# Kernel tuning notes

Hardware: AMD Instinct MI355X
Metric: run time of the kernel (lower is better)

## Reference

```python
import jax, jax.numpy as jnp
import numpy as np
import math

B, S, E = 2, 2048, 1024
H, HD = 16, 64
FF = 4 * E
EPS = float(jnp.finfo(jnp.float32).eps)  # torch nn.RMSNorm default eps


def setup_inputs() -> dict:
    key = jax.random.key(0)
    ks = jax.random.split(key, 20)
    sd = 0.02
    inp = {
        "x": jax.random.normal(ks[0], (B, S, E), jnp.float32),
        "wq": jax.random.normal(ks[1], (E, H * HD), jnp.float32) * sd,
        "bq": jnp.zeros((H * HD,), jnp.float32),
        "wk": jax.random.normal(ks[2], (E, HD), jnp.float32) * sd,
        "bk": jnp.zeros((HD,), jnp.float32),
        "wv": jax.random.normal(ks[3], (E, HD), jnp.float32) * sd,
        "bv": jnp.zeros((HD,), jnp.float32),
        "wo": jax.random.normal(ks[4], (H * HD, E), jnp.float32) * sd,
        "bo": jnp.zeros((E,), jnp.float32),
        "wg": jax.random.normal(ks[5], (E, FF), jnp.float32) * sd,
        "bg": jnp.zeros((FF,), jnp.float32),
        "wu": jax.random.normal(ks[6], (E, FF), jnp.float32) * sd,
        "bu": jnp.zeros((FF,), jnp.float32),
        "wd": jax.random.normal(ks[7], (FF, E), jnp.float32) * sd,
        "bd": jnp.zeros((E,), jnp.float32),
        "g1": jnp.ones((E,), jnp.float32),
        "g2": jnp.ones((E,), jnp.float32),
    }
    return inp


def rmsnorm(x, g):
    ms = jnp.mean(jnp.square(x), axis=-1, keepdims=True)
    return x * jax.lax.rsqrt(ms + EPS) * g


def apply_rope(t):
    # t: [B, H, S, D]; llama-style rotate-half, theta=10000, start_pos=0
    d = t.shape[-1]
    half = d // 2
    inv_freq = 1.0 / (10000.0 ** (jnp.arange(half, dtype=jnp.float32) / half))
    pos = jnp.arange(t.shape[2], dtype=jnp.float32)
    ang = pos[:, None] * inv_freq[None, :]  # [S, half]
    cos, sin = jnp.cos(ang), jnp.sin(ang)
    t1, t2 = t[..., :half], t[..., half:]
    return jnp.concatenate([t1 * cos - t2 * sin, t1 * sin + t2 * cos], axis=-1)


def decoder_fwd(x, wq, bq, wk, bk, wv, bv, wo, bo, wg, bg, wu, bu, wd, bd, g1, g2):
    residual = x
    h = rmsnorm(x, g1)
    # MQA projections: H query heads, 1 shared K/V head
    q = (h @ wq + bq).reshape(B, S, H, HD).transpose(0, 2, 1, 3)  # [B,H,S,D]
    k = (h @ wk + bk)[:, None]                                    # [B,1,S,D]
    v = (h @ wv + bv)                                             # [B,S,D]
    q = apply_rope(q)
    k = apply_rope(k)[:, 0]                                       # [B,S,D]
    scores = jnp.einsum("bhqd,bkd->bhqk", q, k) / math.sqrt(HD)
    causal = jnp.tril(jnp.ones((S, S), dtype=bool))
    scores = jnp.where(causal, scores, -jnp.inf)
    attn = jax.nn.softmax(scores, axis=-1)
    out = jnp.einsum("bhqk,bkd->bhqd", attn, v)
    out = out.transpose(0, 2, 1, 3).reshape(B, S, H * HD)
    x = (out @ wo + bo) + residual
    residual = x
    h = rmsnorm(x, g2)
    gated = jax.nn.gelu(h @ wg + bg, approximate=False)  # torch GELU is exact erf
    up = h @ wu + bu
    x = (up * gated) @ wd + bd
    return x + residual


def reference(x, wq, bq, wk, bk, wv, bv, wo, bo, wg, bg, wu, bu, wd, bd, g1, g2):
    return decoder_fwd(x, wq, bq, wk, bk, wv, bv, wo, bo, wg, bg, wu, bu, wd, bd, g1, g2)
```

## Files before the change

kernel.cpp:

```cpp
#include <hip/hip_runtime.h>
#include <hip/hip_bf16.h>
#include <math.h>

#define BB 2
#define SS 2048
#define EE 1024
#define HH 16
#define HD 64
#define FFF 4096
#define MROWS (BB * SS)
#define EPS_F 1.1920929e-7f
#define NQKV 1152

typedef __hip_bfloat16 bf16;
typedef __attribute__((ext_vector_type(8))) short short8;
typedef __attribute__((ext_vector_type(4))) short short4v;
typedef __attribute__((ext_vector_type(4))) float floatx4;

typedef const __attribute__((address_space(1))) void* gas_t;
typedef __attribute__((address_space(3))) void* las_t;

#define BAR __builtin_amdgcn_s_barrier()
#define WLG do { asm volatile("s_waitcnt lgkmcnt(0)" ::: "memory"); \
                 __builtin_amdgcn_sched_barrier(0); } while (0)
#define VMC(N) asm volatile("s_waitcnt vmcnt(" #N ")" ::: "memory")

__global__ __launch_bounds__(256) void rmsnorm_kernel(const float* __restrict__ x,
                                                      const float* __restrict__ g,
                                                      bf16* __restrict__ out,
                                                      int cols) {
    int row = blockIdx.x;
    const float* xr = x + (size_t)row * cols;
    float ss = 0.0f;
    for (int c = threadIdx.x; c < cols; c += 256) {
        float v = xr[c];
        ss += v * v;
    }
    for (int off = 32; off > 0; off >>= 1) ss += __shfl_xor(ss, off, 64);
    __shared__ float red[4];
    int wave = threadIdx.x >> 6;
    if ((threadIdx.x & 63) == 0) red[wave] = ss;
    __syncthreads();
    float tot = red[0] + red[1] + red[2] + red[3];
    float rs = rsqrtf(tot / (float)cols + EPS_F);
    bf16* orow = out + (size_t)row * cols;
    for (int c = threadIdx.x; c < cols; c += 256) {
        orow[c] = __float2bfloat16(xr[c] * rs * g[c]);
    }
}

__global__ __launch_bounds__(256) void transpose_cast_kernel(const float* __restrict__ W,
                                                             bf16* __restrict__ Wt,
                                                             int K, int N) {
    __shared__ float t[32][33];
    int n0 = blockIdx.x * 32, k0 = blockIdx.y * 32;
    int tx = threadIdx.x & 31, ty = threadIdx.x >> 5;
#pragma unroll
    for (int i = 0; i < 4; ++i) {
        int kk = ty + i * 8;
        t[kk][tx] = W[(size_t)(k0 + kk) * N + n0 + tx];
    }
    __syncthreads();
#pragma unroll
    for (int i = 0; i < 4; ++i) {
        int nn = ty + i * 8;
        Wt[(size_t)(n0 + nn) * K + k0 + tx] = __float2bfloat16(t[tx][nn]);
    }
}

__global__ __launch_bounds__(256) void pack_bqkv_kernel(const float* __restrict__ bq,
                                                        const float* __restrict__ bk,
                                                        const float* __restrict__ bv,
                                                        float* __restrict__ bqkv) {
    int t = blockIdx.x * 256 + threadIdx.x;
    if (t >= NQKV) return;
    float v;
    if (t < 1024)      v = bq[t];
    else if (t < 1088) v = bk[t - 1024];
    else               v = bv[t - 1088];
    bqkv[t] = v;
}

#define GK 64

__global__ __launch_bounds__(256) void gemm_qkv_kernel(
        const bf16* __restrict__ A, const bf16* __restrict__ Bt,
        const float* __restrict__ bias,
        bf16* __restrict__ qout, float* __restrict__ kvout, int K) {
    __shared__ short As[128 * GK];
    __shared__ short Bs[128 * GK];
    int tid = threadIdx.x;
    int wave = tid >> 6, lane = tid & 63;
    int wm = (wave >> 1) * 64, wn = (wave & 1) * 64;
    int row0 = blockIdx.y * 128, col0 = blockIdx.x * 128;
    int lr = lane & 15, lq = lane >> 4;

    int srow = wave * 32 + (lane >> 3);
    int scol = (lane & 7) * 8;
    const bf16* Abase = A + (size_t)(row0 + srow) * K + scol;
    const bf16* Bbase = Bt + (size_t)(col0 + srow) * K + scol;

    floatx4 acc[4][4];
#pragma unroll
    for (int mi = 0; mi < 4; ++mi)
#pragma unroll
        for (int ni = 0; ni < 4; ++ni)
            acc[mi][ni] = (floatx4){0.f, 0.f, 0.f, 0.f};

    for (int k0 = 0; k0 < K; k0 += GK) {
        __syncthreads();
#pragma unroll
        for (int c = 0; c < 4; ++c) {
            __builtin_amdgcn_global_load_lds(
                (gas_t)(Abase + (size_t)(c * 8) * K + k0),
                (las_t)&As[(wave * 32 + c * 8) * GK], 16, 0, 0);
            __builtin_amdgcn_global_load_lds(
                (gas_t)(Bbase + (size_t)(c * 8) * K + k0),
                (las_t)&Bs[(wave * 32 + c * 8) * GK], 16, 0, 0);
        }
        __syncthreads();
#pragma unroll
        for (int ks = 0; ks < GK; ks += 32) {
            short8 af[4], bfr[4];
#pragma unroll
            for (int mi = 0; mi < 4; ++mi)
                af[mi] = *(const short8*)&As[(wm + mi * 16 + lr) * GK + ks + lq * 8];
#pragma unroll
            for (int ni = 0; ni < 4; ++ni)
                bfr[ni] = *(const short8*)&Bs[(wn + ni * 16 + lr) * GK + ks + lq * 8];
#pragma unroll
            for (int mi = 0; mi < 4; ++mi)
#pragma unroll
                for (int ni = 0; ni < 4; ++ni)
                    acc[mi][ni] = __builtin_amdgcn_mfma_f32_16x16x32_bf16(
                        af[mi], bfr[ni], acc[mi][ni], 0, 0, 0);
        }
    }

#pragma unroll
    for (int mi = 0; mi < 4; ++mi) {
#pragma unroll
        for (int ni = 0; ni < 4; ++ni) {
            int gc = col0 + wn + ni * 16 + lr;
            float bv = bias[gc];
#pragma unroll
            for (int r = 0; r < 4; ++r) {
                int gr = row0 + wm + mi * 16 + lq * 4 + r;
                float c = acc[mi][ni][r] + bv;
                if (gc < 1024) qout[(size_t)gr * 1024 + gc] = __float2bfloat16(c);
                else           kvout[(size_t)gr * 128 + (gc - 1024)] = c;
            }
        }
    }
}

__global__ __launch_bounds__(256) void gemm_n64_kernel(
        const bf16* __restrict__ A, const bf16* __restrict__ Bt,
        const float* __restrict__ bias, const float* __restrict__ aux,
        float* __restrict__ C, int M, int N, int K) {
    __shared__ short As[128 * GK];
    __shared__ short Bs[64 * GK];
    int tid = threadIdx.x;
    int wave = tid >> 6, lane = tid & 63;
    int wm = wave * 32;
    int row0 = blockIdx.y * 128, col0 = blockIdx.x * 64;
    int lr = lane & 15, lq = lane >> 4;

    int srow = (lane >> 3);
    int scol = (lane & 7) * 8;
    const bf16* Abase = A + (size_t)(row0 + wave * 32 + srow) * K + scol;
    const bf16* Bbase = Bt + (size_t)(col0 + wave * 16 + srow) * K + scol;

    floatx4 acc[2][4];
#pragma unroll
    for (int mi = 0; mi < 2; ++mi)
#pragma unroll
        for (int ni = 0; ni < 4; ++ni)
            acc[mi][ni] = (floatx4){0.f, 0.f, 0.f, 0.f};

    for (int k0 = 0; k0 < K; k0 += GK) {
        __syncthreads();
#pragma unroll
        for (int c = 0; c < 4; ++c)
            __builtin_amdgcn_global_load_lds(
                (gas_t)(Abase + (size_t)(c * 8) * K + k0),
                (las_t)&As[(wave * 32 + c * 8) * GK], 16, 0, 0);
#pragma unroll
        for (int c = 0; c < 2; ++c)
            __builtin_amdgcn_global_load_lds(
                (gas_t)(Bbase + (size_t)(c * 8) * K + k0),
                (las_t)&Bs[(wave * 16 + c * 8) * GK], 16, 0, 0);
        __syncthreads();
#pragma unroll
        for (int ks = 0; ks < GK; ks += 32) {
            short8 af[2], bfr[4];
#pragma unroll
            for (int mi = 0; mi < 2; ++mi)
                af[mi] = *(const short8*)&As[(wm + mi * 16 + lr) * GK + ks + lq * 8];
#pragma unroll
            for (int ni = 0; ni < 4; ++ni)
                bfr[ni] = *(const short8*)&Bs[(ni * 16 + lr) * GK + ks + lq * 8];
#pragma unroll
            for (int mi = 0; mi < 2; ++mi)
#pragma unroll
                for (int ni = 0; ni < 4; ++ni)
                    acc[mi][ni] = __builtin_amdgcn_mfma_f32_16x16x32_bf16(
                        af[mi], bfr[ni], acc[mi][ni], 0, 0, 0);
        }
    }

#pragma unroll
    for (int mi = 0; mi < 2; ++mi) {
#pragma unroll
        for (int ni = 0; ni < 4; ++ni) {
            int gc = col0 + ni * 16 + lr;
            float bv = bias[gc];
#pragma unroll
            for (int r = 0; r < 4; ++r) {
                int gr = row0 + wm + mi * 16 + lq * 4 + r;
                size_t idx = (size_t)gr * N + gc;
                C[idx] = acc[mi][ni][r] + bv + aux[idx];
            }
        }
    }
}

#define FFN_RD_A(KH, MH) \
    { const short* Ap = &Ab[buf][KH][0]; \
      af[0] = *(const short8*)&Ap[(wr * 128 + ((MH) * 4 + 0) * 16 + lr) * 32 + cs8]; \
      af[1] = *(const short8*)&Ap[(wr * 128 + ((MH) * 4 + 1) * 16 + lr) * 32 + cs8]; \
      af[2] = *(const short8*)&Ap[(wr * 128 + ((MH) * 4 + 2) * 16 + lr) * 32 + cs8]; \
      af[3] = *(const short8*)&Ap[(wr * 128 + ((MH) * 4 + 3) * 16 + lr) * 32 + cs8]; }

#define FFN_RD_B(KH) \
    { const short* Bp = &Bb[buf][KH][0]; \
      gf[0] = *(const short8*)&Bp[(wc * 32 + lr) * 32 + cs8]; \
      gf[1] = *(const short8*)&Bp[(wc * 32 + 16 + lr) * 32 + cs8]; \
      uf[0] = *(const short8*)&Bp[4096 + (wc * 32 + lr) * 32 + cs8]; \
      uf[1] = *(const short8*)&Bp[4096 + (wc * 32 + 16 + lr) * 32 + cs8]; }

#define FFN_MM(MH) \
    __builtin_amdgcn_s_setprio(1); \
    { _Pragma("unroll") for (int mi = 0; mi < 4; ++mi) { \
        ag[(MH) * 4 + mi][0] = __builtin_amdgcn_mfma_f32_16x16x32_bf16(af[mi], gf[0], ag[(MH) * 4 + mi][0], 0, 0, 0); \
        ag[(MH) * 4 + mi][1] = __builtin_amdgcn_mfma_f32_16x16x32_bf16(af[mi], gf[1], ag[(MH) * 4 + mi][1], 0, 0, 0); \
        au[(MH) * 4 + mi][0] = __builtin_amdgcn_mfma_f32_16x16x32_bf16(af[mi], uf[0], au[(MH) * 4 + mi][0], 0, 0, 0); \
        au[(MH) * 4 + mi][1] = __builtin_amdgcn_mfma_f32_16x16x32_bf16(af[mi], uf[1], au[(MH) * 4 + mi][1], 0, 0, 0); } } \
    __builtin_amdgcn_s_setprio(0);

__global__ __launch_bounds__(512, 2) void gemm_ffn_kernel(
        const bf16* __restrict__ A, const bf16* __restrict__ Bg,
        const bf16* __restrict__ Bu, const float* __restrict__ biasg,
        const float* __restrict__ biasu, bf16* __restrict__ C, int K) {
    __shared__ short Ab[2][2][8192];
    __shared__ short Bb[2][2][8192];

    const int tid = threadIdx.x;
    const int w = tid >> 6, lane = tid & 63;
    const int wr = w >> 2, wc = w & 3;
    const int lr = lane & 15, quad = lane >> 4;
    const int row0 = blockIdx.y * 256, col0 = blockIdx.x * 128;
    const int NT = K >> 6;
    const int cs8 = (quad ^ ((lr >> 1) & 3)) * 8;

    const int sr = tid >> 2;
    const int scs = (((tid & 3) ^ ((tid >> 3) & 3))) * 8;

    auto stageA = [&](short* dst, int kcol) {
        __builtin_amdgcn_global_load_lds(
            (gas_t)(A + (size_t)(row0 + sr) * K + kcol + scs),
            (las_t)(dst + tid * 8), 16, 0, 0);
        __builtin_amdgcn_global_load_lds(
            (gas_t)(A + (size_t)(row0 + 128 + sr) * K + kcol + scs),
            (las_t)(dst + 4096 + tid * 8), 16, 0, 0);
    };
    auto stageB = [&](short* dst, int kcol) {
        __builtin_amdgcn_global_load_lds(
            (gas_t)(Bg + (size_t)(col0 + sr) * K + kcol + scs),
            (las_t)(dst + tid * 8), 16, 0, 0);
        __builtin_amdgcn_global_load_lds(
            (gas_t)(Bu + (size_t)(col0 + sr) * K + kcol + scs),
            (las_t)(dst + 4096 + tid * 8), 16, 0, 0);
    };

    floatx4 ag[8][2], au[8][2];
#pragma unroll
    for (int mi = 0; mi < 8; ++mi)
#pragma unroll
        for (int ni = 0; ni < 2; ++ni) {
            ag[mi][ni] = (floatx4){0.f, 0.f, 0.f, 0.f};
            au[mi][ni] = (floatx4){0.f, 0.f, 0.f, 0.f};
        }

    stageA(&Ab[0][0][0], 0);
    stageB(&Bb[0][0][0], 0);
    stageA(&Ab[0][1][0], 32);
    stageB(&Bb[0][1][0], 32);
    stageA(&Ab[1][0][0], 64);
    stageB(&Bb[1][0][0], 64);
    VMC(8);
    BAR;

    for (int k = 0; k < NT; ++k) {
        const int buf = k & 1;
        short8 gf[2], uf[2];
        {
            short8 af[4];
            FFN_RD_A(0, 0)
            FFN_RD_B(0)
            if (k + 1 < NT) stageA(&Ab[buf ^ 1][1][0], (k + 1) * 64 + 32);
            BAR; WLG;
            FFN_MM(0)
            BAR;
        }
        {
            short8 af[4];
            FFN_RD_A(0, 1)
            if (k + 1 < NT) stageB(&Bb[buf ^ 1][1][0], (k + 1) * 64 + 32);
            BAR; WLG;
            FFN_MM(1)
            if (k < NT - 1) { VMC(8); } else { VMC(0); }
            BAR;
        }
        {
            short8 af[4];
            FFN_RD_A(1, 0)
            FFN_RD_B(1)
            if (k + 2 < NT) stageA(&Ab[buf][0][0], (k + 2) * 64);
            BAR; WLG;
            FFN_MM(0)
            BAR;
        }
        {
            short8 af[4];
            FFN_RD_A(1, 1)
            if (k + 2 < NT) stageB(&Bb[buf][0][0], (k + 2) * 64);
            BAR; WLG;
            FFN_MM(1)
            if (k < NT - 2) { VMC(8); } else if (k == NT - 2) { VMC(4); }
            BAR;
        }
    }

#pragma unroll
    for (int mi = 0; mi < 8; ++mi) {
#pragma unroll
        for (int ni = 0; ni < 2; ++ni) {
            int gc = col0 + wc * 32 + ni * 16 + lr;
            float bg_ = biasg[gc], bu_ = biasu[gc];
#pragma unroll
            for (int r = 0; r < 4; ++r) {
                int gr = row0 + wr * 128 + mi * 16 + quad * 4 + r;
                float g = ag[mi][ni][r] + bg_;
                float u = au[mi][ni][r] + bu_;
                float v = 0.5f * g * (1.0f + erff(g * 0.70710678118654752f)) * u;
                C[(size_t)gr * FFF + gc] = __float2bfloat16(v);
            }
        }
    }
}

__global__ __launch_bounds__(256) void rope_table_kernel(float* __restrict__ ct,
                                                         float* __restrict__ st) {
    int idx = blockIdx.x * 256 + threadIdx.x;
    int i = idx & 31, s = idx >> 5;
    float inv = powf(10000.0f, -(float)i / 32.0f);
    float ang = (float)s * inv;
    ct[idx] = cosf(ang);
    st[idx] = sinf(ang);
}

__global__ __launch_bounds__(256) void rope_q_kernel(bf16* __restrict__ t,
                                                     const float* __restrict__ ct,
                                                     const float* __restrict__ st,
                                                     int total) {
    int idx = blockIdx.x * 256 + threadIdx.x;
    if (idx >= total) return;
    int i = idx & 31;
    int h = (idx >> 5) % HH;
    int row = idx / (32 * HH);
    int s = row & (SS - 1);
    float c = ct[s * 32 + i];
    float sn = st[s * 32 + i];
    size_t base = (size_t)row * (HH * HD) + h * 64 + i;
    float t1 = (float)t[base];
    float t2 = (float)t[base + 32];
    t[base]      = __float2bfloat16((t1 * c - t2 * sn) * 0.125f);
    t[base + 32] = __float2bfloat16((t1 * sn + t2 * c) * 0.125f);
}

__global__ __launch_bounds__(256) void prep_kv_kernel(const float* __restrict__ kv,
                                                      const float* __restrict__ ct,
                                                      const float* __restrict__ st,
                                                      bf16* __restrict__ kbf,
                                                      bf16* __restrict__ vtb) {
    __shared__ float vt[64][65];
    int s0 = blockIdx.x * 64;
    int b  = blockIdx.y;
    int tid = threadIdx.x;

    for (int i = tid; i < 2048; i += 256) {
        int sl = i >> 5, ii = i & 31;
        int s = s0 + sl;
        size_t base = ((size_t)(b * SS + s)) * 128;
        float k1 = kv[base + ii], k2 = kv[base + ii + 32];
        float c = ct[s * 32 + ii];
        float sn = st[s * 32 + ii];
        size_t ob = ((size_t)(b * SS + s)) * 64;
        kbf[ob + ii]      = __float2bfloat16(k1 * c - k2 * sn);
        kbf[ob + ii + 32] = __float2bfloat16(k1 * sn + k2 * c);
    }

    for (int i = tid; i < 4096; i += 256) {
        int s = i >> 6, d = i & 63;
        vt[d][s] = kv[((size_t)(b * SS + s0 + s)) * 128 + 64 + d];
    }
    __syncthreads();
    for (int i = tid; i < 4096; i += 256) {
        int d = i >> 6, sl = i & 63;
        vtb[((size_t)(b * 64 + d)) * SS + s0 + sl] = __float2bfloat16(vt[d][sl]);
    }
}

#define PST 68
#define SM_SHIFT 6.0f

__global__ __launch_bounds__(256, 3) void attn_mfma_kernel(
        const bf16* __restrict__ q, const bf16* __restrict__ kb,
        const bf16* __restrict__ vt,
        float* __restrict__ O0p, float* __restrict__ O1p,
        float* __restrict__ l0p, float* __restrict__ l1p) {
    __shared__ short Kb_s[2][64 * 64];
    __shared__ short Vb_s[2][64 * 64];
    __shared__ short Ps[4][16 * PST];

    int h = blockIdx.y, b = blockIdx.z;
    int px = blockIdx.x >> 1, half = blockIdx.x & 1;
    int tid = threadIdx.x, w = tid >> 6, lane = tid & 63;
    int lr = lane & 15, quad = lane >> 4;
    int rsw = lane & 7;

    float* __restrict__ Op = half ? O1p : O0p;
    float* __restrict__ lp = half ? l1p : l0p;

    const bf16* kbB = kb + (size_t)b * SS * 64;
    const bf16* vtB = vt + (size_t)b * 64 * SS;

    int st_sub = lane >> 3;
    int st_col = ((lane & 7) ^ st_sub) << 3;

    auto stage_tile = [&](int nxt, int j0s) {
#pragma unroll
        for (int i = 0; i < 2; ++i) {
            int rr = i * 32 + w * 8 + st_sub;
            __builtin_amdgcn_global_load_lds(
                (gas_t)(kbB + (size_t)(j0s + rr) * 64 + st_col),
                (las_t)&Kb_s[nxt][(i * 256 + w * 64) * 8], 16, 0, 0);
            __builtin_amdgcn_global_load_lds(
                (gas_t)(vtB + (size_t)rr * SS + j0s + st_col),
                (las_t)&Vb_s[nxt][(i * 256 + w * 64) * 8], 16, 0, 0);
        }
    };

    for (int pass = 0; pass < 2; ++pass) {
        int qt = (pass == 0) ? px : (SS / 64 - 1 - px);
        int q0 = qt * 64;

        const bf16* qrow = q + ((size_t)(b * SS + q0 + w * 16 + lr)) * (HH * HD) + h * HD;
        short8 qf0 = *(const short8*)(qrow + quad * 8);
        short8 qf1 = *(const short8*)(qrow + 32 + quad * 8);

        int n  = qt + 1;
        int n0 = (n + 1) >> 1;
        int tlo = half ? n0 : 0;
        int thi = half ? n  : n0;

        floatx4 O[4];
#pragma unroll
        for (int ni = 0; ni < 4; ++ni) O[ni] = (floatx4){0.f, 0.f, 0.f, 0.f};
        float lrow[4] = {0.f, 0.f, 0.f, 0.f};

        int cur = 0;
        if (tlo < thi) stage_tile(0, tlo * 64);
        __syncthreads();

        for (int t = tlo; t < thi; ++t) {
            if (t + 1 < thi) stage_tile(cur ^ 1, (t + 1) * 64);

            int j0 = t * 64;

            floatx4 S[4];
#pragma unroll
            for (int ni = 0; ni < 4; ++ni) S[ni] = (floatx4){0.f, 0.f, 0.f, 0.f};
#pragma unroll
            for (int ni = 0; ni < 4; ++ni) {
                const short* Kc = &Kb_s[cur][(ni * 16 + lr) * 64];
                short8 b0 = *(const short8*)&Kc[(quad ^ rsw) * 8];
                short8 b1 = *(const short8*)&Kc[((quad ^ rsw) ^ 4) * 8];
                S[ni] = __builtin_amdgcn_mfma_f32_16x16x32_bf16(qf0, b0, S[ni], 0, 0, 0);
                S[ni] = __builtin_amdgcn_mfma_f32_16x16x32_bf16(qf1, b1, S[ni], 0, 0, 0);
            }

            short8 vf[8];
#pragma unroll
            for (int ni = 0; ni < 4; ++ni) {
                const short* Vc = &Vb_s[cur][(ni * 16 + lr) * 64];
                vf[2 * ni]     = *(const short8*)&Vc[(quad ^ rsw) * 8];
                vf[2 * ni + 1] = *(const short8*)&Vc[((quad ^ rsw) ^ 4) * 8];
            }

            if (t == qt) {
                int rowg = q0 + w * 16 + quad * 4;
#pragma unroll
                for (int ni = 0; ni < 4; ++ni) {
                    int colg = j0 + ni * 16 + lr;
#pragma unroll
                    for (int r = 0; r < 4; ++r)
                        if (colg > rowg + r) S[ni][r] = -3.0e38f;
                }
            }

#pragma unroll
            for (int ni = 0; ni < 4; ++ni)
#pragma unroll
                for (int r = 0; r < 4; ++r)
                    S[ni][r] = __expf(S[ni][r] - SM_SHIFT);
#pragma unroll
            for (int r = 0; r < 4; ++r)
                lrow[r] += S[0][r] + S[1][r] + S[2][r] + S[3][r];

#pragma unroll
            for (int ni = 0; ni < 4; ++ni)
#pragma unroll
                for (int r = 0; r < 4; ++r) {
                    bf16 pb = __float2bfloat16(S[ni][r]);
                    Ps[w][(quad * 4 + r) * PST + ni * 16 + lr] = *(short*)&pb;
                }
            short4v a0 = *(const short4v*)&Ps[w][lr * PST + quad * 8];
            short4v a1 = *(const short4v*)&Ps[w][lr * PST + quad * 8 + 4];
            short4v a2 = *(const short4v*)&Ps[w][lr * PST + 32 + quad * 8];
            short4v a3 = *(const short4v*)&Ps[w][lr * PST + 32 + quad * 8 + 4];
            short8 p0 = __builtin_shufflevector(a0, a1, 0, 1, 2, 3, 4, 5, 6, 7);
            short8 p1 = __builtin_shufflevector(a2, a3, 0, 1, 2, 3, 4, 5, 6, 7);

#pragma unroll
            for (int ni = 0; ni < 4; ++ni) {
                O[ni] = __builtin_amdgcn_mfma_f32_16x16x32_bf16(p0, vf[2 * ni], O[ni], 0, 0, 0);
                O[ni] = __builtin_amdgcn_mfma_f32_16x16x32_bf16(p1, vf[2 * ni + 1], O[ni], 0, 0, 0);
            }

            __syncthreads();
            cur ^= 1;
        }

#pragma unroll
        for (int r = 0; r < 4; ++r) {
            float l = lrow[r];
            for (int off = 1; off < 16; off <<= 1) l += __shfl_xor(l, off, 64);
            lrow[r] = l;
        }

#pragma unroll
        for (int ni = 0; ni < 4; ++ni) {
            int gc = h * 64 + ni * 16 + lr;
#pragma unroll
            for (int r = 0; r < 4; ++r) {
                int gr = b * SS + q0 + w * 16 + quad * 4 + r;
                Op[(size_t)gr * (HH * HD) + gc] = O[ni][r];
            }
        }
        if (lr == 0) {
#pragma unroll
            for (int r = 0; r < 4; ++r) {
                int gr = b * SS + q0 + w * 16 + quad * 4 + r;
                lp[(size_t)gr * HH + h] = lrow[r];
            }
        }
    }
}

__global__ __launch_bounds__(256) void attn_combine_kernel(
        const float* __restrict__ O0p, const float* __restrict__ O1p,
        const float* __restrict__ l0p, const float* __restrict__ l1p,
        bf16* __restrict__ o) {
    int idx = blockIdx.x * 256 + threadIdx.x;
    int d4  = idx & 15;
    int hh  = (idx >> 4) & 15;
    int row = idx >> 8;
    float l = l0p[row * HH + hh] + l1p[row * HH + hh];
    float inv = 1.0f / l;
    size_t base = (size_t)row * (HH * HD) + hh * 64 + d4 * 4;
    float4 a = *(const float4*)(O0p + base);
    float4 c = *(const float4*)(O1p + base);
    short4v o4;
    {
        bf16 v0 = __float2bfloat16((a.x + c.x) * inv);
        bf16 v1 = __float2bfloat16((a.y + c.y) * inv);
        bf16 v2 = __float2bfloat16((a.z + c.z) * inv);
        bf16 v3 = __float2bfloat16((a.w + c.w) * inv);
        o4[0] = *(short*)&v0; o4[1] = *(short*)&v1;
        o4[2] = *(short*)&v2; o4[3] = *(short*)&v3;
    }
    *(short4v*)(o + base) = o4;
}

#define MB (1024ull * 1024ull)

extern "C" void kernel_launch(void* const* d_in, const int* in_sizes, int n_in,
                              void* d_out, int out_size, void* d_ws, size_t ws_size,
                              hipStream_t stream) {
    const float* x  = (const float*)d_in[0];
    const float* wq = (const float*)d_in[1];
    const float* bq = (const float*)d_in[2];
    const float* wk = (const float*)d_in[3];
    const float* bk = (const float*)d_in[4];
    const float* wv = (const float*)d_in[5];
    const float* bv = (const float*)d_in[6];
    const float* wo = (const float*)d_in[7];
    const float* bo = (const float*)d_in[8];
    const float* wg = (const float*)d_in[9];
    const float* bg = (const float*)d_in[10];
    const float* wu = (const float*)d_in[11];
    const float* bu = (const float*)d_in[12];
    const float* wd = (const float*)d_in[13];
    const float* bd = (const float*)d_in[14];
    const float* g1 = (const float*)d_in[15];
    const float* g2 = (const float*)d_in[16];
    float* out = (float*)d_out;

    char* ws = (char*)d_ws;
    bf16*  qbf   = (bf16*)(ws);
    bf16*  wuT   = (bf16*)(ws + 8 * MB);
    float* x2    = (float*)(ws + 16 * MB);
    bf16*  h1b   = (bf16*)(ws + 32 * MB);
    float* kv    = (float*)(ws + 40 * MB);
    bf16*  ao    = (bf16*)(ws + 42 * MB);
    bf16*  gg    = (bf16*)(ws + 50 * MB);
    bf16*  kbf   = (bf16*)(ws + 50 * MB);
    bf16*  vtb   = (bf16*)(ws + 50 * MB + 512 * 1024);
    float* Opart0 = (float*)(ws + 16 * MB);
    float* Opart1 = (float*)(ws + 51 * MB);
    float* lpart0 = (float*)(ws + 67 * MB);
    float* lpart1 = (float*)(ws + 67 * MB + 256 * 1024);
    float* ctab   = (float*)(ws + 68 * MB);
    float* stab   = (float*)(ws + 68 * MB + 256 * 1024);
    bf16*  wqkvT = (bf16*)(ws + 82 * MB);
    float* bqkv  = (float*)(ws + 84 * MB + 512 * 1024);
    bf16*  woT   = (bf16*)(ws + 85 * MB);
    bf16*  wgT   = (bf16*)(ws);
    bf16*  wdT   = (bf16*)(ws + 42 * MB);
    bf16*  h2b   = h1b;

    rmsnorm_kernel<<<MROWS, 256, 0, stream>>>(x, g1, h1b, EE);

    transpose_cast_kernel<<<dim3(EE / 32, EE / 32), 256, 0, stream>>>(wq, wqkvT, EE, EE);
    transpose_cast_kernel<<<dim3(HD / 32, EE / 32), 256, 0, stream>>>(wk, wqkvT + (size_t)1024 * EE, EE, HD);
    transpose_cast_kernel<<<dim3(HD / 32, EE / 32), 256, 0, stream>>>(wv, wqkvT + (size_t)1088 * EE, EE, HD);
    pack_bqkv_kernel<<<(NQKV + 255) / 256, 256, 0, stream>>>(bq, bk, bv, bqkv);
    transpose_cast_kernel<<<dim3(EE / 32, EE / 32), 256, 0, stream>>>(wo, woT, EE, EE);

    gemm_qkv_kernel<<<dim3(NQKV / 128, MROWS / 128), 256, 0, stream>>>(
        h1b, wqkvT, bqkv, qbf, kv, EE);

    rope_table_kernel<<<(SS * 32) / 256, 256, 0, stream>>>(ctab, stab);

    {
        int total_q = MROWS * HH * 32;
        rope_q_kernel<<<(total_q + 255) / 256, 256, 0, stream>>>(qbf, ctab, stab, total_q);
    }
    prep_kv_kernel<<<dim3(SS / 64, BB), 256, 0, stream>>>(kv, ctab, stab, kbf, vtb);

    attn_mfma_kernel<<<dim3(2 * SS / 128, HH, BB), 256, 0, stream>>>(
        qbf, kbf, vtb, Opart0, Opart1, lpart0, lpart1);
    attn_combine_kernel<<<(MROWS * HH * HD / 4) / 256, 256, 0, stream>>>(
        Opart0, Opart1, lpart0, lpart1, ao);

    gemm_n64_kernel<<<dim3(EE / 64, MROWS / 128), 256, 0, stream>>>(
        ao, woT, bo, x, x2, MROWS, EE, EE);

    rmsnorm_kernel<<<MROWS, 256, 0, stream>>>(x2, g2, h2b, EE);

    transpose_cast_kernel<<<dim3(FFF / 32, EE / 32), 256, 0, stream>>>(wg, wgT, EE, FFF);
    transpose_cast_kernel<<<dim3(FFF / 32, EE / 32), 256, 0, stream>>>(wu, wuT, EE, FFF);

    gemm_ffn_kernel<<<dim3(FFF / 128, MROWS / 256), 512, 0, stream>>>(
        h2b, wgT, wuT, bg, bu, gg, EE);

    transpose_cast_kernel<<<dim3(EE / 32, FFF / 32), 256, 0, stream>>>(wd, wdT, FFF, EE);
    gemm_n64_kernel<<<dim3(EE / 64, MROWS / 128), 256, 0, stream>>>(
        gg, wdT, bd, x2, out, MROWS, EE, FFF);
}
```

Before: 429.0 us.

## Fuse RoPE into QKV GEMM epilogue and batch weight-prep kernels

Applies rotary embedding, including the q scale, directly in the QKV GEMM epilogue. Each wave's 64-column slice is one head, so the rotate-half pairs are already in registers; this removes the separate q RoPE pass and the fp32 K/V intermediate. K and V are now written straight out as bf16, and a slimmer kernel only transposes V. All attention and FFN weight transposes, bias packing and the RoPE table build are merged into two multi-role launches, cutting launch count and small-kernel tail overhead. The trade-off is a heavier, more branchy GEMM epilogue that does scattered cos/sin table loads.

New measurement: 415.3 us. 3.2% less time.

```diff
diff --git a/kernel.cpp b/kernel.cpp
--- a/kernel.cpp
+++ b/kernel.cpp
@@ -49,12 +49,12 @@
     }
 }
 
-__global__ __launch_bounds__(256) void transpose_cast_kernel(const float* __restrict__ W,
-                                                             bf16* __restrict__ Wt,
-                                                             int K, int N) {
-    __shared__ float t[32][33];
-    int n0 = blockIdx.x * 32, k0 = blockIdx.y * 32;
-    int tx = threadIdx.x & 31, ty = threadIdx.x >> 5;
+__device__ __forceinline__ void transpose_tile32(const float* __restrict__ W,
+                                                 bf16* __restrict__ Wt,
+                                                 int K, int N, int bx, int by,
+                                                 int tid, float (*t)[33]) {
+    int n0 = bx * 32, k0 = by * 32;
+    int tx = tid & 31, ty = tid >> 5;
 #pragma unroll
     for (int i = 0; i < 4; ++i) {
         int kk = ty + i * 8;
@@ -68,17 +68,60 @@
     }
 }
 
-__global__ __launch_bounds__(256) void pack_bqkv_kernel(const float* __restrict__ bq,
-                                                        const float* __restrict__ bk,
-                                                        const float* __restrict__ bv,
-                                                        float* __restrict__ bqkv) {
-    int t = blockIdx.x * 256 + threadIdx.x;
-    if (t >= NQKV) return;
-    float v;
-    if (t < 1024)      v = bq[t];
-    else if (t < 1088) v = bk[t - 1024];
-    else               v = bv[t - 1088];
-    bqkv[t] = v;
+__global__ __launch_bounds__(256) void prep_weights_kernel(
+        const float* __restrict__ wq, const float* __restrict__ wk,
+        const float* __restrict__ wv, const float* __restrict__ wo,
+        const float* __restrict__ bq, const float* __restrict__ bk,
+        const float* __restrict__ bv,
+        bf16* __restrict__ wqkvT, bf16* __restrict__ woT,
+        float* __restrict__ bqkv, float* __restrict__ ct, float* __restrict__ st) {
+    __shared__ float t[32][33];
+    int bid = blockIdx.x, tid = threadIdx.x;
+    if (bid < 1024) {
+        transpose_tile32(wq, wqkvT, EE, EE, bid & 31, bid >> 5, tid, t);
+    } else if (bid < 1088) {
+        int b2 = bid - 1024;
+        transpose_tile32(wk, wqkvT + (size_t)1024 * EE, EE, HD, b2 & 1, b2 >> 1, tid, t);
+    } else if (bid < 1152) {
+        int b2 = bid - 1088;
+        transpose_tile32(wv, wqkvT + (size_t)1088 * EE, EE, HD, b2 & 1, b2 >> 1, tid, t);
+    } else if (bid < 2176) {
+        int b2 = bid - 1152;
+        transpose_tile32(wo, woT, EE, EE, b2 & 31, b2 >> 5, tid, t);
+    } else if (bid < 2432) {
+        int idx = (bid - 2176) * 256 + tid;
+        int i = idx & 31, s = idx >> 5;
+        float inv = powf(10000.0f, -(float)i / 32.0f);
+        float ang = (float)s * inv;
+        ct[idx] = cosf(ang);
+        st[idx] = sinf(ang);
+    } else {
+        int tt = (bid - 2432) * 256 + tid;
+        if (tt < NQKV) {
+            float v;
+            if (tt < 1024)      v = bq[tt];
+            else if (tt < 1088) v = bk[tt - 1024];
+            else                v = bv[tt - 1088];
+            bqkv[tt] = v;
+        }
+    }
+}
+
+__global__ __launch_bounds__(256) void ffn_weights_kernel(
+        const float* __restrict__ wg, const float* __restrict__ wu,
+        const float* __restrict__ wd,
+        bf16* __restrict__ wgT, bf16* __restrict__ wuT, bf16* __restrict__ wdT) {
+    __shared__ float t[32][33];
+    int bid = blockIdx.x, tid = threadIdx.x;
+    if (bid < 4096) {
+        transpose_tile32(wg, wgT, EE, FFF, bid & 127, bid >> 7, tid, t);
+    } else if (bid < 8192) {
+        int b2 = bid - 4096;
+        transpose_tile32(wu, wuT, EE, FFF, b2 & 127, b2 >> 7, tid, t);
+    } else {
+        int b2 = bid - 8192;
+        transpose_tile32(wd, wdT, FFF, EE, b2 & 31, b2 >> 5, tid, t);
+    }
 }
 
 #define GK 64
@@ -86,7 +129,9 @@
 __global__ __launch_bounds__(256) void gemm_qkv_kernel(
         const bf16* __restrict__ A, const bf16* __restrict__ Bt,
         const float* __restrict__ bias,
-        bf16* __restrict__ qout, float* __restrict__ kvout, int K) {
+        const float* __restrict__ ct, const float* __restrict__ st,
+        bf16* __restrict__ qout, bf16* __restrict__ kout,
+        bf16* __restrict__ vout, int K) {
     __shared__ short As[128 * GK];
     __shared__ short Bs[128 * GK];
     int tid = threadIdx.x;
@@ -137,20 +182,49 @@
         }
     }
 
-#pragma unroll
-    for (int mi = 0; mi < 4; ++mi) {
-#pragma unroll
-        for (int ni = 0; ni < 4; ++ni) {
-            int gc = col0 + wn + ni * 16 + lr;
-            float bv = bias[gc];
-#pragma unroll
-            for (int r = 0; r < 4; ++r) {
-                int gr = row0 + wm + mi * 16 + lq * 4 + r;
-                float c = acc[mi][ni][r] + bv;
-                if (gc < 1024) qout[(size_t)gr * 1024 + gc] = __float2bfloat16(c);
-                else           kvout[(size_t)gr * 128 + (gc - 1024)] = c;
-            }
-        }
+    int hcol = col0 + wn;
+    if (hcol < 1088) {
+        bool isQ = hcol < 1024;
+#pragma unroll
+        for (int mi = 0; mi < 4; ++mi) {
+#pragma unroll
+            for (int ni = 0; ni < 2; ++ni) {
+                int i = ni * 16 + lr;
+                float b1 = bias[hcol + i];
+                float b2 = bias[hcol + i + 32];
+#pragma unroll
+                for (int r = 0; r < 4; ++r) {
+                    int gr = row0 + wm + mi * 16 + lq * 4 + r;
+                    int s = gr & (SS - 1);
+                    float c  = ct[s * 32 + i];
+                    float sn = st[s * 32 + i];
+                    float t1 = acc[mi][ni][r] + b1;
+                    float t2 = acc[mi][ni + 2][r] + b2;
+                    float o1 = t1 * c - t2 * sn;
+                    float o2 = t1 * sn + t2 * c;
+                    if (isQ) {
+                        qout[(size_t)gr * 1024 + hcol + i]      = __float2bfloat16(o1 * 0.125f);
+                        qout[(size_t)gr * 1024 + hcol + i + 32] = __float2bfloat16(o2 * 0.125f);
+                    } else {
+                        kout[(size_t)gr * 64 + i]      = __float2bfloat16(o1);
+                        kout[(size_t)gr * 64 + i + 32] = __float2bfloat16(o2);
+                    }
+                }
+            }
+        }
+    } else {
+#pragma unroll
+        for (int mi = 0; mi < 4; ++mi)
+#pragma unroll
+            for (int ni = 0; ni < 4; ++ni) {
+                int vcol = ni * 16 + lr;
+                float bv_ = bias[1088 + vcol];
+#pragma unroll
+                for (int r = 0; r < 4; ++r) {
+                    int gr = row0 + wm + mi * 16 + lq * 4 + r;
+                    vout[(size_t)gr * 64 + vcol] = __float2bfloat16(acc[mi][ni][r] + bv_);
+                }
+            }
     }
 }
 
@@ -360,65 +434,21 @@
     }
 }
 
-__global__ __launch_bounds__(256) void rope_table_kernel(float* __restrict__ ct,
-                                                         float* __restrict__ st) {
-    int idx = blockIdx.x * 256 + threadIdx.x;
-    int i = idx & 31, s = idx >> 5;
-    float inv = powf(10000.0f, -(float)i / 32.0f);
-    float ang = (float)s * inv;
-    ct[idx] = cosf(ang);
-    st[idx] = sinf(ang);
-}
-
-__global__ __launch_bounds__(256) void rope_q_kernel(bf16* __restrict__ t,
-                                                     const float* __restrict__ ct,
-                                                     const float* __restrict__ st,
-                                                     int total) {
-    int idx = blockIdx.x * 256 + threadIdx.x;
-    if (idx >= total) return;
-    int i = idx & 31;
-    int h = (idx >> 5) % HH;
-    int row = idx / (32 * HH);
-    int s = row & (SS - 1);
-    float c = ct[s * 32 + i];
-    float sn = st[s * 32 + i];
-    size_t base = (size_t)row * (HH * HD) + h * 64 + i;
-    float t1 = (float)t[base];
-    float t2 = (float)t[base + 32];
-    t[base]      = __float2bfloat16((t1 * c - t2 * sn) * 0.125f);
-    t[base + 32] = __float2bfloat16((t1 * sn + t2 * c) * 0.125f);
-}
-
-__global__ __launch_bounds__(256) void prep_kv_kernel(const float* __restrict__ kv,
-                                                      const float* __restrict__ ct,
-                                                      const float* __restrict__ st,
-                                                      bf16* __restrict__ kbf,
-                                                      bf16* __restrict__ vtb) {
-    __shared__ float vt[64][65];
-    int s0 = blockIdx.x * 64;
-    int b  = blockIdx.y;
+__global__ __launch_bounds__(256) void prep_v_kernel(const bf16* __restrict__ vb,
+                                                     bf16* __restrict__ vtb) {
+    __shared__ short t[64][65];
+    int s0 = blockIdx.x * 64, b = blockIdx.y;
     int tid = threadIdx.x;
-
-    for (int i = tid; i < 2048; i += 256) {
-        int sl = i >> 5, ii = i & 31;
-        int s = s0 + sl;
-        size_t base = ((size_t)(b * SS + s)) * 128;
-        float k1 = kv[base + ii], k2 = kv[base + ii + 32];
-        float c = ct[s * 32 + ii];
-        float sn = st[s * 32 + ii];
-        size_t ob = ((size_t)(b * SS + s)) * 64;
-        kbf[ob + ii]      = __float2bfloat16(k1 * c - k2 * sn);
-        kbf[ob + ii + 32] = __float2bfloat16(k1 * sn + k2 * c);
-    }
-
+    const short* vs = (const short*)vb;
+    short* vd = (short*)vtb;
     for (int i = tid; i < 4096; i += 256) {
         int s = i >> 6, d = i & 63;
-        vt[d][s] = kv[((size_t)(b * SS + s0 + s)) * 128 + 64 + d];
+        t[d][s] = vs[((size_t)(b * SS + s0 + s)) * 64 + d];
     }
     __syncthreads();
     for (int i = tid; i < 4096; i += 256) {
         int d = i >> 6, sl = i & 63;
-        vtb[((size_t)(b * 64 + d)) * SS + s0 + sl] = __float2bfloat16(vt[d][sl]);
+        vd[((size_t)(b * 64 + d)) * SS + s0 + sl] = t[d][sl];
     }
 }
 
@@ -633,7 +663,7 @@
     bf16*  wuT   = (bf16*)(ws + 8 * MB);
     float* x2    = (float*)(ws + 16 * MB);
     bf16*  h1b   = (bf16*)(ws + 32 * MB);
-    float* kv    = (float*)(ws + 40 * MB);
+    bf16*  vb    = (bf16*)(ws + 40 * MB);
     bf16*  ao    = (bf16*)(ws + 42 * MB);
     bf16*  gg    = (bf16*)(ws + 50 * MB);
     bf16*  kbf   = (bf16*)(ws + 50 * MB);
@@ -651,24 +681,15 @@
     bf16*  wdT   = (bf16*)(ws + 42 * MB);
     bf16*  h2b   = h1b;
 
+    prep_weights_kernel<<<2437, 256, 0, stream>>>(
+        wq, wk, wv, wo, bq, bk, bv, wqkvT, woT, bqkv, ctab, stab);
+
     rmsnorm_kernel<<<MROWS, 256, 0, stream>>>(x, g1, h1b, EE);
 
-    transpose_cast_kernel<<<dim3(EE / 32, EE / 32), 256, 0, stream>>>(wq, wqkvT, EE, EE);
-    transpose_cast_kernel<<<dim3(HD / 32, EE / 32), 256, 0, stream>>>(wk, wqkvT + (size_t)1024 * EE, EE, HD);
-    transpose_cast_kernel<<<dim3(HD / 32, EE / 32), 256, 0, stream>>>(wv, wqkvT + (size_t)1088 * EE, EE, HD);
-    pack_bqkv_kernel<<<(NQKV + 255) / 256, 256, 0, stream>>>(bq, bk, bv, bqkv);
-    transpose_cast_kernel<<<dim3(EE / 32, EE / 32), 256, 0, stream>>>(wo, woT, EE, EE);
-
     gemm_qkv_kernel<<<dim3(NQKV / 128, MROWS / 128), 256, 0, stream>>>(
-        h1b, wqkvT, bqkv, qbf, kv, EE);
-
-    rope_table_kernel<<<(SS * 32) / 256, 256, 0, stream>>>(ctab, stab);
-
-    {
-        int total_q = MROWS * HH * 32;
-        rope_q_kernel<<<(total_q + 255) / 256, 256, 0, stream>>>(qbf, ctab, stab, total_q);
-    }
-    prep_kv_kernel<<<dim3(SS / 64, BB), 256, 0, stream>>>(kv, ctab, stab, kbf, vtb);
+        h1b, wqkvT, bqkv, ctab, stab, qbf, kbf, vb, EE);
+
+    prep_v_kernel<<<dim3(SS / 64, BB), 256, 0, stream>>>(vb, vtb);
 
     attn_mfma_kernel<<<dim3(2 * SS / 128, HH, BB), 256, 0, stream>>>(
         qbf, kbf, vtb, Opart0, Opart1, lpart0, lpart1);
@@ -680,13 +701,11 @@
 
     rmsnorm_kernel<<<MROWS, 256, 0, stream>>>(x2, g2, h2b, EE);
 
-    transpose_cast_kernel<<<dim3(FFF / 32, EE / 32), 256, 0, stream>>>(wg, wgT, EE, FFF);
-    transpose_cast_kernel<<<dim3(FFF / 32, EE / 32), 256, 0, stream>>>(wu, wuT, EE, FFF);
+    ffn_weights_kernel<<<12288, 256, 0, stream>>>(wg, wu, wd, wgT, wuT, wdT);
 
     gemm_ffn_kernel<<<dim3(FFF / 128, MROWS / 256), 512, 0, stream>>>(
         h2b, wgT, wuT, bg, bu, gg, EE);
 
-    transpose_cast_kernel<<<dim3(EE / 32, FFF / 32), 256, 0, stream>>>(wd, wdT, FFF, EE);
     gemm_n64_kernel<<<dim3(EE / 64, MROWS / 128), 256, 0, stream>>>(
         gg, wdT, bd, x2, out, MROWS, EE, FFF);
 }
```
